# Kernel tuning notes

Hardware: AMD Instinct MI355X
Metric: run time of the kernel (lower is better)

Reference implementation:

```python
import jax, jax.numpy as jnp
import numpy as np

MIN_SIGMA = 0.1
MAX_SIGMA = 10.0


def _sigma_mlp(e, w1, b1, w2, b2, w3, b3):
    # e: [B, N, E] -> sigma in [min_sigma, max_sigma], shape [B, N, 1]
    h = jax.nn.gelu(e @ w1 + b1, approximate=False)
    h = jax.nn.gelu(h @ w2 + b2, approximate=False)
    s = jax.nn.sigmoid(h @ w3 + b3)
    return MIN_SIGMA + (MAX_SIGMA - MIN_SIGMA) * s


def setup_inputs() -> dict:
    key = jax.random.key(0)
    ks = jax.random.split(key, 9)
    M, P = 2048, 2
    B, N, E = 8, 1024, 256
    H = 32
    z = jax.random.normal(ks[0], (M, P), dtype=jnp.float32)
    mu = jax.random.normal(ks[1], (B, N, P), dtype=jnp.float32)
    embeddings = jax.random.normal(ks[2], (B, N, E), dtype=jnp.float32)
    # sigma-predictor MLP params (torch Linear default-ish init scale)
    w1 = jax.random.normal(ks[3], (E, H), dtype=jnp.float32) / np.sqrt(E)
    b1 = jnp.zeros((H,), dtype=jnp.float32)
    w2 = jax.random.normal(ks[4], (H, H // 2), dtype=jnp.float32) / np.sqrt(H)
    b2 = jnp.zeros((H // 2,), dtype=jnp.float32)
    w3 = jax.random.normal(ks[5], (H // 2, 1), dtype=jnp.float32) / np.sqrt(H // 2)
    b3 = jnp.zeros((1,), dtype=jnp.float32)
    return {"z": z, "mu": mu, "embeddings": embeddings,
            "w1": w1, "b1": b1, "w2": w2, "b2": b2, "w3": w3, "b3": b3}


def reference(z, mu, embeddings, w1, b1, w2, b2, w3, b3):
    # sigma: [B, N, 1]
    sigma = _sigma_mlp(embeddings, w1, b1, w2, b2, w3, b3)
    # squared distances: [B, N, M] = sum_P (z[m,p] - mu[b,n,p])^2
    # z: [M, P], mu: [B, N, P]
    d2 = jnp.sum((z[None, None, :, :] - mu[:, :, None, :]) ** 2, axis=-1)
    # kernel values: [B, N, M]
    return jnp.exp(-d2 / (2.0 * sigma ** 2))
```

## Files before the change

### kernel.cpp

```cpp
#include <hip/hip_runtime.h>
#include <math.h>

#define ROWS 8192
#define M_TOTAL 2048
#define E_DIM 256
#define H1 32
#define H2 16

__device__ __forceinline__ float gelu_exact(float x) {
    return 0.5f * x * (1.0f + erff(x * 0.70710678118654752f));
}

__global__ __launch_bounds__(256) void fused_rbf(
    const float* __restrict__ z, const float* __restrict__ mu,
    const float* __restrict__ emb,
    const float* __restrict__ w1, const float* __restrict__ b1,
    const float* __restrict__ w2, const float* __restrict__ b2,
    const float* __restrict__ w3, const float* __restrict__ b3,
    float* __restrict__ out)
{
    __shared__ __align__(16) float sh1p[32 * 32];
    __shared__ float sh1[H1];
    __shared__ float sh2[H2];
    __shared__ float sc;

    const int t = threadIdx.x;
    const int row = blockIdx.x;

    const float mu0 = mu[row * 2 + 0];
    const float mu1 = mu[row * 2 + 1];
    const float4* zf4 = (const float4*)z;
    float d2[8];
    #pragma unroll
    for (int i = 0; i < 2; ++i) {
        const int idx = i * 256 + t;
        const float4 za = zf4[idx * 2 + 0];
        const float4 zb = zf4[idx * 2 + 1];
        float a, b;
        a = za.x - mu0; b = za.y - mu1; d2[i * 4 + 0] = fmaf(b, b, a * a);
        a = za.z - mu0; b = za.w - mu1; d2[i * 4 + 1] = fmaf(b, b, a * a);
        a = zb.x - mu0; b = zb.y - mu1; d2[i * 4 + 2] = fmaf(b, b, a * a);
        a = zb.z - mu0; b = zb.w - mu1; d2[i * 4 + 3] = fmaf(b, b, a * a);
    }

    {
        const int og = t & 7;
        const int kg = t >> 3;
        const float4* e4 = (const float4*)(emb + (size_t)row * E_DIM);
        const float4 e0 = e4[kg * 2 + 0];
        const float4 e1 = e4[kg * 2 + 1];
        const float ev[8] = {e0.x, e0.y, e0.z, e0.w, e1.x, e1.y, e1.z, e1.w};
        const float4* w14 = (const float4*)w1;
        float4 p = make_float4(0.f, 0.f, 0.f, 0.f);
        #pragma unroll
        for (int kk = 0; kk < 8; ++kk) {
            const float4 w = w14[(kg * 8 + kk) * 8 + og];
            p.x = fmaf(ev[kk], w.x, p.x);
            p.y = fmaf(ev[kk], w.y, p.y);
            p.z = fmaf(ev[kk], w.z, p.z);
            p.w = fmaf(ev[kk], w.w, p.w);
        }
        ((float4*)sh1p)[t] = p;
    }
    __syncthreads();

    if (t < H1) {
        float a = 0.f;
        #pragma unroll
        for (int kg = 0; kg < 32; ++kg) a += sh1p[kg * 32 + t];
        sh1[t] = gelu_exact(a + b1[t]);
    }
    if (t < H2) {
        float a = 0.f;
        #pragma unroll
        for (int k = 0; k < H1; ++k) a = fmaf(sh1[k], w2[k * H2 + t], a);
        sh2[t] = gelu_exact(a + b2[t]);
    }
    if (t == 0) {
        float s = 0.f;
        #pragma unroll
        for (int k = 0; k < H2; ++k) s = fmaf(sh2[k], w3[k], s);
        const float x = s + b3[0];
        const float sig = 1.0f / (1.0f + __expf(-x));
        const float sigma = 0.1f + 9.9f * sig;
        sc = -0.5f / (sigma * sigma);
    }
    __syncthreads();

    const float c = sc;
    float4* out4 = (float4*)out + (size_t)row * (M_TOTAL / 4);
    #pragma unroll
    for (int i = 0; i < 2; ++i) {
        const int idx = i * 256 + t;
        float4 r;
        r.x = __expf(d2[i * 4 + 0] * c);
        r.y = __expf(d2[i * 4 + 1] * c);
        r.z = __expf(d2[i * 4 + 2] * c);
        r.w = __expf(d2[i * 4 + 3] * c);
        out4[idx] = r;
    }
}

extern "C" void kernel_launch(void* const* d_in, const int* in_sizes, int n_in,
                              void* d_out, int out_size, void* d_ws, size_t ws_size,
                              hipStream_t stream) {
    const float* z   = (const float*)d_in[0];
    const float* mu  = (const float*)d_in[1];
    const float* emb = (const float*)d_in[2];
    const float* w1  = (const float*)d_in[3];
    const float* b1  = (const float*)d_in[4];
    const float* w2  = (const float*)d_in[5];
    const float* b2  = (const float*)d_in[6];
    const float* w3  = (const float*)d_in[7];
    const float* b3  = (const float*)d_in[8];
    float* out = (float*)d_out;

    fused_rbf<<<ROWS, 256, 0, stream>>>(z, mu, emb, w1, b1, w2, b2, w3, b3, out);
}
```

Measured before the change: 108.7 us.

## Process eight rows per block to reuse z and w1 registers

Each block now handles eight rows instead of one, so z and the w1 slice are loaded into registers once and reused across rows. The MLP stages are parallelised across the eight rows, with padded shared-memory partial sums to avoid bank conflicts. This cuts per-block setup, global reloads of z and w1, and barrier overhead relative to the output write. The cost is fewer blocks (1024), more registers per thread, and more shared memory per block, which may lower occupancy and latency hiding for the output stores.

```diff
diff --git a/kernel.cpp b/kernel.cpp
--- a/kernel.cpp
+++ b/kernel.cpp
@@ -6,12 +6,14 @@
 #define E_DIM 256
 #define H1 32
 #define H2 16
+#define R_PER_BLK 8
+#define NBLK (ROWS / R_PER_BLK)
 
 __device__ __forceinline__ float gelu_exact(float x) {
     return 0.5f * x * (1.0f + erff(x * 0.70710678118654752f));
 }
 
-__global__ __launch_bounds__(256) void fused_rbf(
+__global__ __launch_bounds__(256) void fused_rbf_r8(
     const float* __restrict__ z, const float* __restrict__ mu,
     const float* __restrict__ emb,
     const float* __restrict__ w1, const float* __restrict__ b1,
@@ -19,85 +21,95 @@
     const float* __restrict__ w3, const float* __restrict__ b3,
     float* __restrict__ out)
 {
-    __shared__ __align__(16) float sh1p[32 * 32];
-    __shared__ float sh1[H1];
-    __shared__ float sh2[H2];
-    __shared__ float sc;
+    __shared__ __align__(16) float part[R_PER_BLK * 32 * 36];
+    __shared__ float sh1[R_PER_BLK * 33];
+    __shared__ float sh2[R_PER_BLK * 17];
+    __shared__ float sc[R_PER_BLK];
 
     const int t = threadIdx.x;
-    const int row = blockIdx.x;
+    const int row0 = blockIdx.x * R_PER_BLK;
 
-    const float mu0 = mu[row * 2 + 0];
-    const float mu1 = mu[row * 2 + 1];
-    const float4* zf4 = (const float4*)z;
-    float d2[8];
+    const float4* z4 = (const float4*)z;
+    const float4 za0 = z4[(size_t)t * 2 + 0];
+    const float4 zb0 = z4[(size_t)t * 2 + 1];
+    const float4 za1 = z4[(size_t)(256 + t) * 2 + 0];
+    const float4 zb1 = z4[(size_t)(256 + t) * 2 + 1];
+
+    const int og = t & 7;
+    const int kg = t >> 3;
+    const float4* w14 = (const float4*)w1;
+    float4 w[8];
     #pragma unroll
-    for (int i = 0; i < 2; ++i) {
-        const int idx = i * 256 + t;
-        const float4 za = zf4[idx * 2 + 0];
-        const float4 zb = zf4[idx * 2 + 1];
-        float a, b;
-        a = za.x - mu0; b = za.y - mu1; d2[i * 4 + 0] = fmaf(b, b, a * a);
-        a = za.z - mu0; b = za.w - mu1; d2[i * 4 + 1] = fmaf(b, b, a * a);
-        a = zb.x - mu0; b = zb.y - mu1; d2[i * 4 + 2] = fmaf(b, b, a * a);
-        a = zb.z - mu0; b = zb.w - mu1; d2[i * 4 + 3] = fmaf(b, b, a * a);
-    }
+    for (int kk = 0; kk < 8; ++kk) w[kk] = w14[(kg * 8 + kk) * 8 + og];
 
-    {
-        const int og = t & 7;
-        const int kg = t >> 3;
-        const float4* e4 = (const float4*)(emb + (size_t)row * E_DIM);
+    #pragma unroll
+    for (int r = 0; r < R_PER_BLK; ++r) {
+        const float4* e4 = (const float4*)(emb + (size_t)(row0 + r) * E_DIM);
         const float4 e0 = e4[kg * 2 + 0];
         const float4 e1 = e4[kg * 2 + 1];
         const float ev[8] = {e0.x, e0.y, e0.z, e0.w, e1.x, e1.y, e1.z, e1.w};
-        const float4* w14 = (const float4*)w1;
         float4 p = make_float4(0.f, 0.f, 0.f, 0.f);
         #pragma unroll
         for (int kk = 0; kk < 8; ++kk) {
-            const float4 w = w14[(kg * 8 + kk) * 8 + og];
-            p.x = fmaf(ev[kk], w.x, p.x);
-            p.y = fmaf(ev[kk], w.y, p.y);
-            p.z = fmaf(ev[kk], w.z, p.z);
-            p.w = fmaf(ev[kk], w.w, p.w);
+            p.x = fmaf(ev[kk], w[kk].x, p.x);
+            p.y = fmaf(ev[kk], w[kk].y, p.y);
+            p.z = fmaf(ev[kk], w[kk].z, p.z);
+            p.w = fmaf(ev[kk], w[kk].w, p.w);
         }
-        ((float4*)sh1p)[t] = p;
+        *(float4*)&part[r * (32 * 36) + kg * 36 + og * 4] = p;
     }
     __syncthreads();
 
-    if (t < H1) {
+    {
+        const int r = t >> 5;
+        const int o = t & 31;
         float a = 0.f;
         #pragma unroll
-        for (int kg = 0; kg < 32; ++kg) a += sh1p[kg * 32 + t];
-        sh1[t] = gelu_exact(a + b1[t]);
-    }
-    if (t < H2) {
-        float a = 0.f;
-        #pragma unroll
-        for (int k = 0; k < H1; ++k) a = fmaf(sh1[k], w2[k * H2 + t], a);
-        sh2[t] = gelu_exact(a + b2[t]);
-    }
-    if (t == 0) {
-        float s = 0.f;
-        #pragma unroll
-        for (int k = 0; k < H2; ++k) s = fmaf(sh2[k], w3[k], s);
-        const float x = s + b3[0];
-        const float sig = 1.0f / (1.0f + __expf(-x));
-        const float sigma = 0.1f + 9.9f * sig;
-        sc = -0.5f / (sigma * sigma);
+        for (int g = 0; g < 32; ++g) a += part[r * (32 * 36) + g * 36 + o];
+        sh1[r * 33 + o] = gelu_exact(a + b1[o]);
     }
     __syncthreads();
 
-    const float c = sc;
-    float4* out4 = (float4*)out + (size_t)row * (M_TOTAL / 4);
+    if (t < 64) {
+        #pragma unroll
+        for (int h = 0; h < 2; ++h) {
+            const int r = (t >> 4) + 4 * h;
+            const int o2 = t & 15;
+            float a = 0.f;
+            #pragma unroll
+            for (int k = 0; k < H1; ++k) a = fmaf(sh1[r * 33 + k], w2[k * H2 + o2], a);
+            sh2[r * 17 + o2] = gelu_exact(a + b2[o2]);
+        }
+        if (t < R_PER_BLK) {
+            float s = 0.f;
+            #pragma unroll
+            for (int k = 0; k < H2; ++k) s = fmaf(sh2[t * 17 + k], w3[k], s);
+            const float x = s + b3[0];
+            const float sig = 1.0f / (1.0f + __expf(-x));
+            const float sigma = 0.1f + 9.9f * sig;
+            sc[t] = -0.5f / (sigma * sigma);
+        }
+    }
+    __syncthreads();
+
     #pragma unroll
-    for (int i = 0; i < 2; ++i) {
-        const int idx = i * 256 + t;
-        float4 r;
-        r.x = __expf(d2[i * 4 + 0] * c);
-        r.y = __expf(d2[i * 4 + 1] * c);
-        r.z = __expf(d2[i * 4 + 2] * c);
-        r.w = __expf(d2[i * 4 + 3] * c);
-        out4[idx] = r;
+    for (int r = 0; r < R_PER_BLK; ++r) {
+        const float c = sc[r];
+        const float mu0 = mu[(size_t)(row0 + r) * 2 + 0];
+        const float mu1 = mu[(size_t)(row0 + r) * 2 + 1];
+        float4* out4 = (float4*)out + (size_t)(row0 + r) * (M_TOTAL / 4);
+        float a, b;
+        float4 r0, r1;
+        a = za0.x - mu0; b = za0.y - mu1; r0.x = __expf(fmaf(b, b, a * a) * c);
+        a = za0.z - mu0; b = za0.w - mu1; r0.y = __expf(fmaf(b, b, a * a) * c);
+        a = zb0.x - mu0; b = zb0.y - mu1; r0.z = __expf(fmaf(b, b, a * a) * c);
+        a = zb0.z - mu0; b = zb0.w - mu1; r0.w = __expf(fmaf(b, b, a * a) * c);
+        a = za1.x - mu0; b = za1.y - mu1; r1.x = __expf(fmaf(b, b, a * a) * c);
+        a = za1.z - mu0; b = za1.w - mu1; r1.y = __expf(fmaf(b, b, a * a) * c);
+        a = zb1.x - mu0; b = zb1.y - mu1; r1.z = __expf(fmaf(b, b, a * a) * c);
+        a = zb1.z - mu0; b = zb1.w - mu1; r1.w = __expf(fmaf(b, b, a * a) * c);
+        out4[t] = r0;
+        out4[256 + t] = r1;
     }
 }
 
@@ -115,5 +127,5 @@
     const float* b3  = (const float*)d_in[8];
     float* out = (float*)d_out;
 
-    fused_rbf<<<ROWS, 256, 0, stream>>>(z, mu, emb, w1, b1, w2, b2, w3, b3, out);
+    fused_rbf_r8<<<NBLK, 256, 0, stream>>>(z, mu, emb, w1, b1, w2, b2, w3, b3, out);
 }
```

After: 99.23 us. 1.09x faster.
